# Optimization experiments

Hardware: AMD Instinct MI355X
Metric: run time of the kernel (lower is better)

## Reference

```python
import jax, jax.numpy as jnp
import numpy as np

NEG = -1e12


def setup_inputs() -> dict:
    key = jax.random.key(0)
    ks = jax.random.split(key, 10)
    B, C, Q, D = 16, 384, 64, 2048
    return {
        "c": jax.random.normal(ks[0], (B, C, D), dtype=jnp.float32),
        "q": jax.random.normal(ks[1], (B, Q, D), dtype=jnp.float32),
        "c_len": jax.random.randint(ks[2], (B,), 1, C + 1),
        "q_len": jax.random.randint(ks[3], (B,), 1, Q + 1),
        "w_c": jax.random.normal(ks[4], (D,), dtype=jnp.float32) * 0.02,
        "b_c": jnp.zeros((), dtype=jnp.float32),
        "w_q": jax.random.normal(ks[5], (D,), dtype=jnp.float32) * 0.02,
        "b_q": jnp.zeros((), dtype=jnp.float32),
        "w_cq": jax.random.normal(ks[6], (D,), dtype=jnp.float32) * 0.02,
        "b_cq": jnp.zeros((), dtype=jnp.float32),
        "W_out": jax.random.normal(ks[7], (4 * D, 2), dtype=jnp.float32) * 0.02,
        "b_out": jnp.zeros((2,), dtype=jnp.float32),
    }


def reference(c, q, c_len, q_len, w_c, b_c, w_q, b_q, w_cq, b_cq, W_out, b_out):
    B, C, D = c.shape
    Q = q.shape[1]
    # trilinear similarity: s[b,r,i] = w_c.c_r + w_q.q_i + w_cq.(c_r*q_i) + biases
    cq = jnp.einsum('bcd,bqd,d->bcq', c, q, w_cq) + b_cq          # [B,C,Q]
    s = (c @ w_c + b_c)[:, :, None] + (q @ w_q + b_q)[:, None, :] + cq
    rows = jnp.arange(C)[None, :, None]
    cols = jnp.arange(Q)[None, None, :]
    # faithful to the triple loop: cols >= q_len OR (rows >= c_len AND col < Q-1)
    masked = (cols >= q_len[:, None, None]) | (
        (rows >= c_len[:, None, None]) & (cols < Q - 1))
    s = s + jnp.where(masked, jnp.float32(NEG), jnp.float32(0.0))
    a = jax.nn.softmax(s, axis=2)                                  # [B,C,Q]
    c2q = jnp.einsum('bcq,bqd->bcd', a, q)                         # [B,C,D]
    b_att = jax.nn.softmax(jnp.max(s, axis=2), axis=1)             # [B,C]
    q2c = jnp.einsum('bc,bcd->bd', b_att, c)[:, None, :]           # [B,1,D]
    x = jnp.concatenate(
        [c, c2q, c * c2q, c * jnp.broadcast_to(q2c, c.shape)], axis=-1)
    out = x @ W_out + b_out                                        # [B,C,2]
    # final masking: out[i][c_len[i]:-1] = NEG (last row untouched)
    row_mask = (jnp.arange(C)[None, :] >= c_len[:, None]) & (
        jnp.arange(C)[None, :] < C - 1)
    out = jnp.where(row_mask[..., None], jnp.float32(NEG), out)
    return out[..., 0], out[..., 1]
```

## Files before the change

kernel.cpp:

```cpp
#include <hip/hip_runtime.h>

#define NEGV -1.0e12f
constexpr int B = 16, C = 384, Q = 64, D = 2048;
constexpr int PITCH = 40;
constexpr int IST = 8320;
constexpr int NT = 96;
constexpr int KC = 4;
constexpr int SP = 208;

typedef __attribute__((ext_vector_type(8))) short s16x8;
typedef __attribute__((ext_vector_type(4))) float f32x4;

__device__ __forceinline__ unsigned pkbf(float lo, float hi) {
  unsigned ulo = __builtin_bit_cast(unsigned, lo);
  unsigned uhi = __builtin_bit_cast(unsigned, hi);
  return (uhi & 0xFFFF0000u) | (ulo >> 16);
}
__device__ __forceinline__ float bflo(unsigned u) {
  return __builtin_bit_cast(float, u << 16);
}
__device__ __forceinline__ float bfhi(unsigned u) {
  return __builtin_bit_cast(float, u & 0xFFFF0000u);
}
__device__ __forceinline__ float bfs(unsigned short u) {
  return __builtin_bit_cast(float, ((unsigned)u) << 16);
}

#define GLD_LDS(gsrc, ldst)                                              \
  __builtin_amdgcn_global_load_lds(                                      \
      (const __attribute__((address_space(1))) unsigned*)(gsrc),         \
      (__attribute__((address_space(3))) unsigned*)(ldst), 16, 0, 0)

__global__ __launch_bounds__(256) void k_prep(
    const float* __restrict__ q, const float* __restrict__ w_q,
    const float* __restrict__ w_cq, const float* __restrict__ w_c,
    const float* __restrict__ W_out, float* __restrict__ qstats,
    float* __restrict__ wpack) {
  const int t = threadIdx.x;
  if (blockIdx.x < 1024) {
    int bi = blockIdx.x;
    const float* qrow = q + (size_t)bi * D;
    float a0 = 0.f, a1 = 0.f, a2 = 0.f;
    for (int d = t * 4; d < D; d += 256 * 4) {
      float4 qv = *(const float4*)(qrow + d);
      float4 wq = *(const float4*)(w_q + d);
      const float* wp = W_out + (size_t)(D + d) * 2;
      float4 wa = *(const float4*)(wp);
      float4 wb = *(const float4*)(wp + 4);
      a0 += qv.x * wq.x + qv.y * wq.y + qv.z * wq.z + qv.w * wq.w;
      a1 += qv.x * wa.x + qv.y * wa.z + qv.z * wb.x + qv.w * wb.z;
      a2 += qv.x * wa.y + qv.y * wa.w + qv.z * wb.y + qv.w * wb.w;
    }
    for (int m = 1; m < 64; m <<= 1) {
      a0 += __shfl_xor(a0, m, 64);
      a1 += __shfl_xor(a1, m, 64);
      a2 += __shfl_xor(a2, m, 64);
    }
    __shared__ float red[3][4];
    int w = t >> 6, lane = t & 63;
    if (lane == 0) { red[0][w] = a0; red[1][w] = a1; red[2][w] = a2; }
    __syncthreads();
    if (t == 0) {
      qstats[bi * 3 + 0] = red[0][0] + red[0][1] + red[0][2] + red[0][3];
      qstats[bi * 3 + 1] = red[1][0] + red[1][1] + red[1][2] + red[1][3];
      qstats[bi * 3 + 2] = red[2][0] + red[2][1] + red[2][2] + red[2][3];
    }
  } else {
    int wb = blockIdx.x - 1024;
    int plane = wb >> 1, half = wb & 1;
    int k = half * 1024 + t * 4;
    float4 v;
    if (plane == 0) {
      v = *(const float4*)(w_cq + k);
    } else if (plane == 3) {
      v = *(const float4*)(w_c + k);
    } else {
      const float* s;
      if (plane == 1)
        s = W_out + (size_t)(2 * D + k) * 2;
      else if (plane == 2)
        s = W_out + (size_t)(2 * D + k) * 2 + 1;
      else if (plane == 4)
        s = W_out + (size_t)k * 2;
      else
        s = W_out + (size_t)k * 2 + 1;
      v = make_float4(s[0], s[2], s[4], s[6]);
    }
    *(float4*)(wpack + plane * 2048 + k) = v;
  }
}

__global__ __launch_bounds__(512, 1) void k_score(
    const float* __restrict__ wpack, const float* __restrict__ q,
    const float* __restrict__ c, unsigned short* __restrict__ S3pb,
    unsigned short* __restrict__ cbf) {
  const int t = threadIdx.x;
  const int lane = t & 63, wv = t >> 6;
  const int bid = blockIdx.x;
  const int b = bid & 15, kcb = (bid >> 4) & 3, n0 = (bid >> 6) * NT;
  const int lr = lane & 15, lg = lane >> 4;
  const int mg = wv >> 1, ng = wv & 1;

  __shared__ unsigned short sBp[4][IST];
  __shared__ unsigned short sCp[4][NT * PITCH];
  __shared__ float wL[6 * 512];

  {
    int p = t >> 7, j4 = (t & 127) * 4;
    GLD_LDS(wpack + p * 2048 + kcb * 512 + j4, wL + p * 512 + j4);
    if (t < 256) {
      int c2 = 512 + t;
      int p2 = c2 >> 7, k4 = (c2 & 127) * 4;
      GLD_LDS(wpack + p2 * 2048 + kcb * 512 + k4, wL + p2 * 512 + k4);
    }
  }
  asm volatile("s_waitcnt vmcnt(0)" ::: "memory");
  __builtin_amdgcn_s_barrier();

  const float* cbase = c + ((size_t)b * C + n0) * D + kcb * 512;
  unsigned short* cbf_base = cbf + ((size_t)b * C + n0) * D + kcb * 512;
  const int qi = t >> 3, qkc = (t & 7) * 4;
  const float* qbase = q + ((size_t)b * Q + qi) * D + kcb * 512 + qkc;

  f32x4 acc[4][3];
#pragma unroll
  for (int f = 0; f < 4; ++f)
#pragma unroll
    for (int g = 0; g < 3; ++g) acc[f][g] = f32x4{0.f, 0.f, 0.f, 0.f};

  auto loadQ = [&](float4& r, int s) {
    r = *(const float4*)(qbase + s * 32);
  };
  auto loadC = [&](float4* r, int s) {
    const float* base = cbase + s * 32;
    if (wv < 4) {
      int g0 = wv * 128 + lane;
      r[0] = *(const float4*)(base + (size_t)(g0 >> 3) * D + (g0 & 7) * 4);
      int g1 = g0 + 64;
      r[1] = *(const float4*)(base + (size_t)(g1 >> 3) * D + (g1 & 7) * 4);
    } else {
      int g0 = 512 + (wv - 4) * 64 + lane;
      r[0] = *(const float4*)(base + (size_t)(g0 >> 3) * D + (g0 & 7) * 4);
    }
  };
  auto writeB = [&](int buf, const float4& rq, int s) {
    int ko = s * 32 + qkc;
    float4 w0 = *(const float4*)&wL[ko];
    float4 w1 = *(const float4*)&wL[512 + ko];
    float4 w2 = *(const float4*)&wL[1024 + ko];
    uint2 u;
    u.x = pkbf(rq.x * w0.x, rq.y * w0.y);
    u.y = pkbf(rq.z * w0.z, rq.w * w0.w);
    *(uint2*)&sBp[buf][qi * PITCH + qkc] = u;
    u.x = pkbf(rq.x * w1.x, rq.y * w1.y);
    u.y = pkbf(rq.z * w1.z, rq.w * w1.w);
    *(uint2*)&sBp[buf][(64 + qi) * PITCH + qkc] = u;
    u.x = pkbf(rq.x * w2.x, rq.y * w2.y);
    u.y = pkbf(rq.z * w2.z, rq.w * w2.w);
    *(uint2*)&sBp[buf][(128 + qi) * PITCH + qkc] = u;
    if (t < 24) {
      int r = t >> 3, kc2 = (t & 7) * 4;
      float4 wv4 = *(const float4*)&wL[(3 + r) * 512 + s * 32 + kc2];
      uint2 us;
      us.x = pkbf(wv4.x, wv4.y);
      us.y = pkbf(wv4.z, wv4.w);
      *(uint2*)&sBp[buf][(192 + r) * PITCH + kc2] = us;
    }
  };
  auto writeC = [&](int buf, const float4* r, int s) {
    unsigned short* cb = cbf_base + s * 32;
    if (wv < 4) {
      int g0 = wv * 128 + lane;
      uint2 u0 = {pkbf(r[0].x, r[0].y), pkbf(r[0].z, r[0].w)};
      *(uint2*)&sCp[buf][(g0 >> 3) * PITCH + (g0 & 7) * 4] = u0;
      *(uint2*)(cb + (size_t)(g0 >> 3) * D + (g0 & 7) * 4) = u0;
      int g1 = g0 + 64;
      uint2 u1 = {pkbf(r[1].x, r[1].y), pkbf(r[1].z, r[1].w)};
      *(uint2*)&sCp[buf][(g1 >> 3) * PITCH + (g1 & 7) * 4] = u1;
      *(uint2*)(cb + (size_t)(g1 >> 3) * D + (g1 & 7) * 4) = u1;
    } else {
      int g0 = 512 + (wv - 4) * 64 + lane;
      uint2 u0 = {pkbf(r[0].x, r[0].y), pkbf(r[0].z, r[0].w)};
      *(uint2*)&sCp[buf][(g0 >> 3) * PITCH + (g0 & 7) * 4] = u0;
      *(uint2*)(cb + (size_t)(g0 >> 3) * D + (g0 & 7) * 4) = u0;
    }
  };
  auto compute = [&](int buf) {
    s16x8 af[4], bf[3];
#pragma unroll
    for (int f = 0; f < 4; ++f)
      af[f] = *(const s16x8*)&sBp[buf][(mg * 64 + f * 16 + lr) * PITCH +
                                       lg * 8];
#pragma unroll
    for (int g = 0; g < 3; ++g)
      bf[g] = *(const s16x8*)&sCp[buf][((ng * 3 + g) * 16 + lr) * PITCH +
                                       lg * 8];
#pragma unroll
    for (int f = 0; f < 4; ++f)
#pragma unroll
      for (int g = 0; g < 3; ++g)
        acc[f][g] =
            __builtin_amdgcn_mfma_f32_16x16x32_bf16(af[f], bf[g], acc[f][g],
                                                    0, 0, 0);
  };

  auto vmwait2 = [&]() {
    if (wv < 4)
      asm volatile("s_waitcnt vmcnt(10)" ::: "memory");
    else
      asm volatile("s_waitcnt vmcnt(6)" ::: "memory");
  };
  auto vmwait1 = [&]() {
    if (wv < 4)
      asm volatile("s_waitcnt vmcnt(7)" ::: "memory");
    else
      asm volatile("s_waitcnt vmcnt(4)" ::: "memory");
  };
  auto vmwait0 = [&]() {
    if (wv < 4)
      asm volatile("s_waitcnt vmcnt(4)" ::: "memory");
    else
      asm volatile("s_waitcnt vmcnt(2)" ::: "memory");
  };

  float4 rc[4][2], rq[4];
  loadC(rc[0], 0);
  loadQ(rq[0], 0);
  loadC(rc[1], 1);
  loadQ(rq[1], 1);
#pragma unroll
  for (int s = 0; s < 16; ++s) {
    const int cur = s & 3;
    if (s + 2 < 16) {
      loadC(rc[(s + 2) & 3], s + 2);
      loadQ(rq[(s + 2) & 3], s + 2);
      vmwait2();
    } else if (s + 1 < 16) {
      vmwait1();
    } else {
      vmwait0();
    }
    writeB(cur, rq[cur], s);
    writeC(cur, rc[cur], s);
    asm volatile("s_waitcnt lgkmcnt(0)" ::: "memory");
    __builtin_amdgcn_sched_barrier(0);
    __builtin_amdgcn_s_barrier();
    compute(cur);
  }

  const size_t rowbase = ((size_t)kcb * B + b) * C;
#pragma unroll
  for (int f = 0; f < 4; ++f) {
    int mf = mg * 4 + f;
    if (mf < 13) {
#pragma unroll
      for (int g = 0; g < 3; ++g) {
        int n = n0 + (ng * 3 + g) * 16 + lr;
        uint2 pk;
        pk.x = pkbf(acc[f][g][0], acc[f][g][1]);
        pk.y = pkbf(acc[f][g][2], acc[f][g][3]);
        *(uint2*)(S3pb + (rowbase + n) * SP + mf * 16 + lg * 4) = pk;
      }
    }
  }
}

__global__ __launch_bounds__(256) void k_soft(
    const unsigned short* __restrict__ S3pb, const float* __restrict__ qstats,
    const int* __restrict__ c_len, const int* __restrict__ q_len,
    const float* __restrict__ b_c, const float* __restrict__ b_q,
    const float* __restrict__ b_cq, float* __restrict__ mrow,
    float* __restrict__ out12) {
  const int t = threadIdx.x, lane = t & 63;
  const int rg = blockIdx.x * 4 + (t >> 6);
  const int b = rg / C, r = rg % C;
  float s_cq = 0.f, sc = 0.f, w10 = 0.f, w11 = 0.f, t30 = 0.f, t31 = 0.f;
#pragma unroll
  for (int p = 0; p < KC; ++p) {
    const unsigned short* Sr = S3pb + ((size_t)p * B * C + rg) * SP;
    s_cq += bfs(Sr[lane]);
    sc += bfs(Sr[192]);
    w10 += bfs(Sr[193]);
    w11 += bfs(Sr[194]);
    t30 += bfs(Sr[64 + lane]);
    t31 += bfs(Sr[128 + lane]);
  }
  const float qs0 = qstats[((b << 6) + lane) * 3 + 0];
  const float qs1 = qstats[((b << 6) + lane) * 3 + 1];
  const float qs2 = qstats[((b << 6) + lane) * 3 + 2];
  float s = s_cq + sc + qs0 + b_c[0] + b_q[0] + b_cq[0];
  const int cl = c_len[b], ql = q_len[b];
  bool masked = (lane >= ql) || ((r >= cl) && (lane < Q - 1));
  if (masked) s += NEGV;
  float mx = s;
  for (int m = 1; m < 64; m <<= 1) mx = fmaxf(mx, __shfl_xor(mx, m, 64));
  float e = __expf(s - mx);
  float den = e;
  for (int m = 1; m < 64; m <<= 1) den += __shfl_xor(den, m, 64);
  float a = e / den;
  float v0 = a * (qs1 + t30);
  float v1 = a * (qs2 + t31);
  for (int m = 1; m < 64; m <<= 1) {
    v0 += __shfl_xor(v0, m, 64);
    v1 += __shfl_xor(v1, m, 64);
  }
  if (lane == 0) {
    mrow[rg] = mx;
    out12[rg * 2 + 0] = w10 + v0;
    out12[rg * 2 + 1] = w11 + v1;
  }
}

__global__ __launch_bounds__(512) void k_q2cu(
    const unsigned short* __restrict__ cbf, const float* __restrict__ mrow,
    const float* __restrict__ W_out, float* __restrict__ uvec) {
  const int ch = blockIdx.x, b = blockIdx.y;
  const int t = threadIdx.x, lane = t & 63, wv = t >> 6;
  __shared__ float batt[C];
  __shared__ float rmx[8], rsm[8];
  __shared__ float redq0[8][64], redq1[8][64];

  float m = (t < C) ? mrow[b * C + t] : -3.0e38f;
  float mx = m;
  for (int o = 1; o < 64; o <<= 1) mx = fmaxf(mx, __shfl_xor(mx, o, 64));
  if (lane == 0) rmx[wv] = mx;
  __syncthreads();
  mx = rmx[0];
#pragma unroll
  for (int i = 1; i < 8; ++i) mx = fmaxf(mx, rmx[i]);
  float e = (t < C) ? __expf(m - mx) : 0.f;
  float sm = e;
  for (int o = 1; o < 64; o <<= 1) sm += __shfl_xor(sm, o, 64);
  if (lane == 0) rsm[wv] = sm;
  __syncthreads();
  sm = rsm[0] + rsm[1] + rsm[2] + rsm[3] + rsm[4] + rsm[5] + rsm[6] + rsm[7];
  if (t < C) batt[t] = e / sm;
  __syncthreads();

  const int d0 = ch * 128 + lane * 2;
  const unsigned short* p = cbf + ((size_t)b * C + wv * 8) * D + d0;
  float A0[8] = {0.f, 0.f, 0.f, 0.f, 0.f, 0.f, 0.f, 0.f};
  float A1[8] = {0.f, 0.f, 0.f, 0.f, 0.f, 0.f, 0.f, 0.f};
#pragma unroll
  for (int r0 = 0; r0 < 384; r0 += 64) {
    const unsigned short* pr = p + (size_t)r0 * D;
    const float* bt = &batt[r0 + wv * 8];
#pragma unroll
    for (int j = 0; j < 8; ++j) {
      unsigned cc = *(const unsigned*)(pr + (size_t)j * D);
      A0[j] += bt[j] * bflo(cc);
      A1[j] += bt[j] * bfhi(cc);
    }
  }
  float s0 = ((A0[0] + A0[1]) + (A0[2] + A0[3])) +
             ((A0[4] + A0[5]) + (A0[6] + A0[7]));
  float s1 = ((A1[0] + A1[1]) + (A1[2] + A1[3])) +
             ((A1[4] + A1[5]) + (A1[6] + A1[7]));
  redq0[wv][lane] = s0;
  redq1[wv][lane] = s1;
  __syncthreads();
  if (t < 64) {
    float q0 = 0.f, q1 = 0.f;
#pragma unroll
    for (int w = 0; w < 8; ++w) {
      q0 += redq0[w][t];
      q1 += redq1[w][t];
    }
    int dd = ch * 128 + t * 2;
    float4 w4 = *(const float4*)(W_out + (size_t)(3 * D + dd) * 2);
    float4 u = {q0 * w4.x, q0 * w4.y, q1 * w4.z, q1 * w4.w};
    *(float4*)(uvec + ((size_t)b * D + dd) * 2) = u;
  }
}

__global__ __launch_bounds__(512) void k_out(
    const unsigned short* __restrict__ cbf, const float* __restrict__ uvec,
    const float* __restrict__ out12, const float* __restrict__ b_out,
    const int* __restrict__ c_len, float* __restrict__ outp) {
  const int b = blockIdx.y, r0 = blockIdx.x * 8;
  const int t = threadIdx.x, lane = t & 63, wv = t >> 6;
  __shared__ float u_sh[2 * D];

  {
    const float* src = uvec + (size_t)b * D * 2 + t * 8;
    float4 v0 = *(const float4*)(src);
    float4 v1 = *(const float4*)(src + 4);
    *(float4*)&u_sh[t * 8] = v0;
    *(float4*)&u_sh[t * 8 + 4] = v1;
  }
  __syncthreads();

  const int r = r0 + wv;
  const unsigned short* crow = cbf + ((size_t)b * C + r) * D;
  float o0 = 0.f, o1 = 0.f;
#pragma unroll
  for (int it = 0; it < 16; ++it) {
    int d0 = it * 128 + lane * 2;
    unsigned cc = *(const unsigned*)(crow + d0);
    float c0 = bflo(cc), c1 = bfhi(cc);
    float4 u = *(const float4*)&u_sh[d0 * 2];
    o0 += c0 * u.x + c1 * u.z;
    o1 += c0 * u.y + c1 * u.w;
  }
  for (int o = 1; o < 64; o <<= 1) {
    o0 += __shfl_xor(o0, o, 64);
    o1 += __shfl_xor(o1, o, 64);
  }
  if (lane == 0) {
    const int idx = b * C + r;
    o0 += out12[idx * 2 + 0] + b_out[0];
    o1 += out12[idx * 2 + 1] + b_out[1];
    if (r >= c_len[b] && r < C - 1) { o0 = NEGV; o1 = NEGV; }
    outp[idx] = o0;
    outp[B * C + idx] = o1;
  }
}

extern "C" void kernel_launch(void* const* d_in, const int* in_sizes, int n_in,
                              void* d_out, int out_size, void* d_ws,
                              size_t ws_size, hipStream_t stream) {
  const float* c = (const float*)d_in[0];
  const float* q = (const float*)d_in[1];
  const int* c_len = (const int*)d_in[2];
  const int* q_len = (const int*)d_in[3];
  const float* w_c = (const float*)d_in[4];
  const float* b_c = (const float*)d_in[5];
  const float* w_q = (const float*)d_in[6];
  const float* b_q = (const float*)d_in[7];
  const float* w_cq = (const float*)d_in[8];
  const float* b_cq = (const float*)d_in[9];
  const float* W_out = (const float*)d_in[10];
  const float* b_out = (const float*)d_in[11];
  float* outp = (float*)d_out;

  float* wpack = (float*)d_ws;
  unsigned short* S3pb = (unsigned short*)(wpack + 6 * 2048);
  const size_t s3_elems = (size_t)KC * B * C * SP;
  float* ws = (float*)(S3pb + s3_elems);
  float* qstats = ws;
  float* mrow = ws + 3072;
  float* out12 = ws + 3072 + 6144;
  float* uvec = ws + 3072 + 6144 + 12288;
  unsigned short* cbf = (unsigned short*)(uvec + 65536);

  hipLaunchKernelGGL(k_prep, dim3(1024 + 12), dim3(256), 0, stream, q, w_q,
                     w_cq, w_c, W_out, qstats, wpack);
  hipLaunchKernelGGL(k_score, dim3(4 * KC * B), dim3(512), 0, stream, wpack,
                     q, c, S3pb, cbf);
  hipLaunchKernelGGL(k_soft, dim3(B * C / 4), dim3(256), 0, stream, S3pb,
                     qstats, c_len, q_len, b_c, b_q, b_cq, mrow, out12);
  hipLaunchKernelGGL(k_q2cu, dim3(16, B), dim3(512), 0, stream, cbf, mrow,
                     W_out, uvec);
  hipLaunchKernelGGL(k_out, dim3(C / 8, B), dim3(512), 0, stream, cbf, uvec,
                     out12, b_out, c_len, outp);
}
```

Baseline: 43.92 us.

## Fold q-stats and weight packing into score kernel, drop prep launch

Removes the separate k_prep kernel. The score kernel now loads and de-interleaves the weight slices straight from the inputs into LDS. It also computes per-kc partial q·w_q and q·W_out dot products from the q tiles it already loads, and k_soft sums those partials. This saves one kernel launch and a second full read of q, at the cost of extra LDS reads and FMAs in the score kernel's staging step, and the weights are now loaded with scalar reads.

```diff
diff --git a/kernel.cpp b/kernel.cpp
--- a/kernel.cpp
+++ b/kernel.cpp
@@ -26,96 +26,40 @@
   return __builtin_bit_cast(float, ((unsigned)u) << 16);
 }
 
-#define GLD_LDS(gsrc, ldst)                                              \
-  __builtin_amdgcn_global_load_lds(                                      \
-      (const __attribute__((address_space(1))) unsigned*)(gsrc),         \
-      (__attribute__((address_space(3))) unsigned*)(ldst), 16, 0, 0)
-
-__global__ __launch_bounds__(256) void k_prep(
-    const float* __restrict__ q, const float* __restrict__ w_q,
+__global__ __launch_bounds__(512, 1) void k_score(
+    const float* __restrict__ q, const float* __restrict__ c,
     const float* __restrict__ w_cq, const float* __restrict__ w_c,
-    const float* __restrict__ W_out, float* __restrict__ qstats,
-    float* __restrict__ wpack) {
-  const int t = threadIdx.x;
-  if (blockIdx.x < 1024) {
-    int bi = blockIdx.x;
-    const float* qrow = q + (size_t)bi * D;
-    float a0 = 0.f, a1 = 0.f, a2 = 0.f;
-    for (int d = t * 4; d < D; d += 256 * 4) {
-      float4 qv = *(const float4*)(qrow + d);
-      float4 wq = *(const float4*)(w_q + d);
-      const float* wp = W_out + (size_t)(D + d) * 2;
-      float4 wa = *(const float4*)(wp);
-      float4 wb = *(const float4*)(wp + 4);
-      a0 += qv.x * wq.x + qv.y * wq.y + qv.z * wq.z + qv.w * wq.w;
-      a1 += qv.x * wa.x + qv.y * wa.z + qv.z * wb.x + qv.w * wb.z;
-      a2 += qv.x * wa.y + qv.y * wa.w + qv.z * wb.y + qv.w * wb.w;
-    }
-    for (int m = 1; m < 64; m <<= 1) {
-      a0 += __shfl_xor(a0, m, 64);
-      a1 += __shfl_xor(a1, m, 64);
-      a2 += __shfl_xor(a2, m, 64);
-    }
-    __shared__ float red[3][4];
-    int w = t >> 6, lane = t & 63;
-    if (lane == 0) { red[0][w] = a0; red[1][w] = a1; red[2][w] = a2; }
-    __syncthreads();
-    if (t == 0) {
-      qstats[bi * 3 + 0] = red[0][0] + red[0][1] + red[0][2] + red[0][3];
-      qstats[bi * 3 + 1] = red[1][0] + red[1][1] + red[1][2] + red[1][3];
-      qstats[bi * 3 + 2] = red[2][0] + red[2][1] + red[2][2] + red[2][3];
-    }
-  } else {
-    int wb = blockIdx.x - 1024;
-    int plane = wb >> 1, half = wb & 1;
-    int k = half * 1024 + t * 4;
-    float4 v;
-    if (plane == 0) {
-      v = *(const float4*)(w_cq + k);
-    } else if (plane == 3) {
-      v = *(const float4*)(w_c + k);
-    } else {
-      const float* s;
-      if (plane == 1)
-        s = W_out + (size_t)(2 * D + k) * 2;
-      else if (plane == 2)
-        s = W_out + (size_t)(2 * D + k) * 2 + 1;
-      else if (plane == 4)
-        s = W_out + (size_t)k * 2;
-      else
-        s = W_out + (size_t)k * 2 + 1;
-      v = make_float4(s[0], s[2], s[4], s[6]);
-    }
-    *(float4*)(wpack + plane * 2048 + k) = v;
-  }
-}
-
-__global__ __launch_bounds__(512, 1) void k_score(
-    const float* __restrict__ wpack, const float* __restrict__ q,
-    const float* __restrict__ c, unsigned short* __restrict__ S3pb,
-    unsigned short* __restrict__ cbf) {
+    const float* __restrict__ w_q, const float* __restrict__ W_out,
+    unsigned short* __restrict__ S3pb, unsigned short* __restrict__ cbf,
+    float* __restrict__ qstatsP) {
   const int t = threadIdx.x;
   const int lane = t & 63, wv = t >> 6;
   const int bid = blockIdx.x;
-  const int b = bid & 15, kcb = (bid >> 4) & 3, n0 = (bid >> 6) * NT;
+  const int b = bid & 15, kcb = (bid >> 4) & 3, n0g = bid >> 6;
+  const int n0 = n0g * NT;
   const int lr = lane & 15, lg = lane >> 4;
   const int mg = wv >> 1, ng = wv & 1;
 
   __shared__ unsigned short sBp[4][IST];
   __shared__ unsigned short sCp[4][NT * PITCH];
-  __shared__ float wL[6 * 512];
+  __shared__ float wL[9 * 512];
 
   {
-    int p = t >> 7, j4 = (t & 127) * 4;
-    GLD_LDS(wpack + p * 2048 + kcb * 512 + j4, wL + p * 512 + j4);
-    if (t < 256) {
-      int c2 = 512 + t;
-      int p2 = c2 >> 7, k4 = (c2 & 127) * 4;
-      GLD_LDS(wpack + p2 * 2048 + kcb * 512 + k4, wL + p2 * 512 + k4);
-    }
-  }
-  asm volatile("s_waitcnt vmcnt(0)" ::: "memory");
-  __builtin_amdgcn_s_barrier();
+    const int k = kcb * 512 + t;
+    wL[t] = w_cq[k];
+    wL[3 * 512 + t] = w_c[k];
+    wL[6 * 512 + t] = w_q[k];
+    float2 v3 = *(const float2*)(W_out + (size_t)(2 * D + k) * 2);
+    wL[512 + t] = v3.x;
+    wL[1024 + t] = v3.y;
+    float2 v1 = *(const float2*)(W_out + (size_t)k * 2);
+    wL[4 * 512 + t] = v1.x;
+    wL[5 * 512 + t] = v1.y;
+    float2 v2 = *(const float2*)(W_out + (size_t)(D + k) * 2);
+    wL[7 * 512 + t] = v2.x;
+    wL[8 * 512 + t] = v2.y;
+  }
+  __syncthreads();
 
   const float* cbase = c + ((size_t)b * C + n0) * D + kcb * 512;
   unsigned short* cbf_base = cbf + ((size_t)b * C + n0) * D + kcb * 512;
@@ -127,6 +71,7 @@
   for (int f = 0; f < 4; ++f)
 #pragma unroll
     for (int g = 0; g < 3; ++g) acc[f][g] = f32x4{0.f, 0.f, 0.f, 0.f};
+  float aq0 = 0.f, aq1 = 0.f, aq2 = 0.f;
 
   auto loadQ = [&](float4& r, int s) {
     r = *(const float4*)(qbase + s * 32);
@@ -158,6 +103,12 @@
     u.x = pkbf(rq.x * w2.x, rq.y * w2.y);
     u.y = pkbf(rq.z * w2.z, rq.w * w2.w);
     *(uint2*)&sBp[buf][(128 + qi) * PITCH + qkc] = u;
+    float4 w6 = *(const float4*)&wL[6 * 512 + ko];
+    float4 w7 = *(const float4*)&wL[7 * 512 + ko];
+    float4 w8 = *(const float4*)&wL[8 * 512 + ko];
+    aq0 += rq.x * w6.x + rq.y * w6.y + rq.z * w6.z + rq.w * w6.w;
+    aq1 += rq.x * w7.x + rq.y * w7.y + rq.z * w7.z + rq.w * w7.w;
+    aq2 += rq.x * w8.x + rq.y * w8.y + rq.z * w8.z + rq.w * w8.w;
     if (t < 24) {
       int r = t >> 3, kc2 = (t & 7) * 4;
       float4 wv4 = *(const float4*)&wL[(3 + r) * 512 + s * 32 + kc2];
@@ -248,6 +199,18 @@
     compute(cur);
   }
 
+  for (int m = 1; m < 8; m <<= 1) {
+    aq0 += __shfl_xor(aq0, m, 64);
+    aq1 += __shfl_xor(aq1, m, 64);
+    aq2 += __shfl_xor(aq2, m, 64);
+  }
+  if (n0g == 0 && (t & 7) == 0) {
+    float* p = qstatsP + (((size_t)kcb * B + b) * Q + qi) * 3;
+    p[0] = aq0;
+    p[1] = aq1;
+    p[2] = aq2;
+  }
+
   const size_t rowbase = ((size_t)kcb * B + b) * C;
 #pragma unroll
   for (int f = 0; f < 4; ++f) {
@@ -266,7 +229,7 @@
 }
 
 __global__ __launch_bounds__(256) void k_soft(
-    const unsigned short* __restrict__ S3pb, const float* __restrict__ qstats,
+    const unsigned short* __restrict__ S3pb, const float* __restrict__ qstatsP,
     const int* __restrict__ c_len, const int* __restrict__ q_len,
     const float* __restrict__ b_c, const float* __restrict__ b_q,
     const float* __restrict__ b_cq, float* __restrict__ mrow,
@@ -275,6 +238,7 @@
   const int rg = blockIdx.x * 4 + (t >> 6);
   const int b = rg / C, r = rg % C;
   float s_cq = 0.f, sc = 0.f, w10 = 0.f, w11 = 0.f, t30 = 0.f, t31 = 0.f;
+  float qs0 = 0.f, qs1 = 0.f, qs2 = 0.f;
 #pragma unroll
   for (int p = 0; p < KC; ++p) {
     const unsigned short* Sr = S3pb + ((size_t)p * B * C + rg) * SP;
@@ -284,10 +248,11 @@
     w11 += bfs(Sr[194]);
     t30 += bfs(Sr[64 + lane]);
     t31 += bfs(Sr[128 + lane]);
-  }
-  const float qs0 = qstats[((b << 6) + lane) * 3 + 0];
-  const float qs1 = qstats[((b << 6) + lane) * 3 + 1];
-  const float qs2 = qstats[((b << 6) + lane) * 3 + 2];
+    const float* qp = qstatsP + (((size_t)p * B + b) * Q + lane) * 3;
+    qs0 += qp[0];
+    qs1 += qp[1];
+    qs2 += qp[2];
+  }
   float s = s_cq + sc + qs0 + b_c[0] + b_q[0] + b_cq[0];
   const int cl = c_len[b], ql = q_len[b];
   bool masked = (lane >= ql) || ((r >= cl) && (lane < Q - 1));
@@ -433,22 +398,19 @@
   const float* b_out = (const float*)d_in[11];
   float* outp = (float*)d_out;
 
-  float* wpack = (float*)d_ws;
-  unsigned short* S3pb = (unsigned short*)(wpack + 6 * 2048);
+  unsigned short* S3pb = (unsigned short*)d_ws;
   const size_t s3_elems = (size_t)KC * B * C * SP;
   float* ws = (float*)(S3pb + s3_elems);
-  float* qstats = ws;
-  float* mrow = ws + 3072;
-  float* out12 = ws + 3072 + 6144;
-  float* uvec = ws + 3072 + 6144 + 12288;
+  float* qstatsP = ws;
+  float* mrow = ws + 12288;
+  float* out12 = ws + 12288 + 6144;
+  float* uvec = ws + 12288 + 6144 + 12288;
   unsigned short* cbf = (unsigned short*)(uvec + 65536);
 
-  hipLaunchKernelGGL(k_prep, dim3(1024 + 12), dim3(256), 0, stream, q, w_q,
-                     w_cq, w_c, W_out, qstats, wpack);
-  hipLaunchKernelGGL(k_score, dim3(4 * KC * B), dim3(512), 0, stream, wpack,
-                     q, c, S3pb, cbf);
+  hipLaunchKernelGGL(k_score, dim3(4 * KC * B), dim3(512), 0, stream, q, c,
+                     w_cq, w_c, w_q, W_out, S3pb, cbf, qstatsP);
   hipLaunchKernelGGL(k_soft, dim3(B * C / 4), dim3(256), 0, stream, S3pb,
-                     qstats, c_len, q_len, b_c, b_q, b_cq, mrow, out12);
+                     qstatsP, c_len, q_len, b_c, b_q, b_cq, mrow, out12);
   hipLaunchKernelGGL(k_q2cu, dim3(16, B), dim3(512), 0, stream, cbf, mrow,
                      W_out, uvec);
   hipLaunchKernelGGL(k_out, dim3(C / 8, B), dim3(512), 0, stream, cbf, uvec,
```

New measurement: 57.27 us. 1.3x slower.
